# Kernel tuning notes

Hardware: AMD Instinct MI355X
Metric: run time of the kernel (lower is better)

## Reference

```python
import jax, jax.numpy as jnp
import numpy as np

N_HEAD = 8
D_HEAD = 64
D_MODEL = 512
CTX = 64
B = 2
Q_LEN = 2048
T = Q_LEN + CTX - 1


def setup_inputs() -> dict:
    key = jax.random.key(0)
    ks = jax.random.split(key, 7)
    HD = N_HEAD * D_HEAD
    return {
        "x": jax.random.normal(ks[0], (B, T, D_MODEL), jnp.float32),
        "r": jax.random.normal(ks[1], (CTX, D_MODEL), jnp.float32),
        "Wkv": jax.random.normal(ks[2], (D_MODEL, 2 * HD), jnp.float32) * 0.02,
        "Wq": jax.random.normal(ks[3], (D_MODEL, HD), jnp.float32) * 0.02,
        "bq": jax.random.normal(ks[4], (HD,), jnp.float32) * 0.02,
        "Wr": jax.random.normal(ks[5], (D_MODEL, HD), jnp.float32) * 0.02,
        "Wo": jax.random.normal(ks[6], (HD, D_MODEL), jnp.float32) * 0.02,
    }


def reference(x, r, Wkv, Wq, bq, Wr, Wo):
    Bb, Tt, _ = x.shape
    C = r.shape[0]
    H, Dh = N_HEAD, D_HEAD
    q_len = Tt - C + 1
    scale = Dh ** -0.5

    kv = x @ Wkv                                  # [B, T, 2*H*Dh]
    k_all = kv[..., : H * Dh].reshape(Bb, Tt, H, Dh)
    v_all = kv[..., H * Dh:].reshape(Bb, Tt, H, Dh)

    # sliding windows (torch unfold(1, ctx, 1) equivalent)
    idx = jnp.arange(q_len)[:, None] + jnp.arange(C)[None, :]   # [q, C]
    k_win = k_all[:, idx]                         # [B, q, C, H, Dh]
    v_win = v_all[:, idx]                         # [B, q, C, H, Dh]

    hq = (x[:, C - 1:] @ Wq + bq).reshape(Bb, q_len, H, Dh)     # [B, q, H, Dh]
    hr = (r @ Wr).reshape(C, H, Dh)                              # [C, H, Dh]

    # q . (k + r): split into content term + relative-position bias term
    scores = (jnp.einsum('bqhd,bqchd->bhqc', hq, k_win)
              + jnp.einsum('bqhd,chd->bhqc', hq, hr)) * scale    # [B, H, q, C]

    # padding mask: positions in first ctx-1 steps that are all-zero
    pad_mask = jnp.all(x[:, : C - 1] == 0, axis=-1)              # [B, C-1]
    full_mask = jnp.concatenate(
        [pad_mask, jnp.zeros((Bb, q_len), dtype=bool)], axis=1)  # [B, T]
    mask_win = full_mask[:, idx]                                 # [B, q, C]
    scores = jnp.where(mask_win[:, None], -jnp.inf, scores)

    w = jax.nn.softmax(scores, axis=-1)                          # [B, H, q, C]
    out = jnp.einsum('bhqc,bqchd->bqhd', w, v_win).reshape(Bb, q_len, H * Dh)
    return out @ Wo                                              # [B, q, d_model]
```

## Files before the change

### kernel.cpp

```cpp
#include <hip/hip_runtime.h>
#include <cstdint>
#include <cstddef>

#define NH 8
#define DH 64
#define DM 512
#define CTX 64
#define BB 2
#define QL 2048
#define TT (QL + CTX - 1)
#define HDIM 512
#define KVN 1024
#define KD 512

typedef unsigned short u16;
typedef __attribute__((ext_vector_type(8))) short bf16x8;
typedef __attribute__((ext_vector_type(4))) float f32x4;

__device__ __forceinline__ u16 f2bf(float f) {
    uint32_t u = __float_as_uint(f);
    u += 0x7FFF + ((u >> 16) & 1);
    return (u16)(u >> 16);
}
__device__ __forceinline__ uint32_t packbf(float lo, float hi) {
    return (uint32_t)f2bf(lo) | ((uint32_t)f2bf(hi) << 16);
}

#define GLLDS(g, l) __builtin_amdgcn_global_load_lds( \
    (const __attribute__((address_space(1))) void*)(g), \
    (__attribute__((address_space(3))) void*)(l), 16, 0, 0)

__global__ __launch_bounds__(256) void prep_kernel(
    const float* __restrict__ Wkv, const float* __restrict__ Wq,
    const float* __restrict__ Wr, const float* __restrict__ Wo,
    u16* __restrict__ WkvqT, u16* __restrict__ WrT, u16* __restrict__ WoT)
{
    __shared__ float tile[64][65];
    const int bid = blockIdx.x;
    const int tid = threadIdx.x;

    const float* W; u16* WT; int N; int tidx;
    if (bid < 128)      { W = Wkv; WT = WkvqT;                    N = 1024; tidx = bid; }
    else if (bid < 192) { W = Wq;  WT = WkvqT + (size_t)1024*512; N = 512;  tidx = bid - 128; }
    else if (bid < 256) { W = Wr;  WT = WrT;                      N = 512;  tidx = bid - 192; }
    else                { W = Wo;  WT = WoT;                      N = 512;  tidx = bid - 256; }
    const int tpr = N / 64;
    const int kb = (tidx / tpr) * 64, nb = (tidx % tpr) * 64;
    const int c4 = (tid & 15) * 4;
    for (int kk = tid >> 4; kk < 64; kk += 16) {
        float4 v = *(const float4*)&W[(size_t)(kb + kk) * N + nb + c4];
        tile[kk][c4 + 0] = v.x; tile[kk][c4 + 1] = v.y;
        tile[kk][c4 + 2] = v.z; tile[kk][c4 + 3] = v.w;
    }
    __syncthreads();
    for (int nn = tid >> 4; nn < 64; nn += 16) {
        ushort4 o;
        o.x = f2bf(tile[c4 + 0][nn]); o.y = f2bf(tile[c4 + 1][nn]);
        o.z = f2bf(tile[c4 + 2][nn]); o.w = f2bf(tile[c4 + 3][nn]);
        *(ushort4*)&WT[(size_t)(nb + nn) * KD + kb + c4] = o;
    }
}

__global__ __launch_bounds__(256) void gemm_fused(
    const float* __restrict__ x, const u16* __restrict__ WkvqT,
    u16* __restrict__ kvb, u16* __restrict__ hqb, const float* __restrict__ bq,
    const float* __restrict__ r, const u16* __restrict__ WrT,
    u16* __restrict__ hrb, float* __restrict__ maskv)
{
    const int bid = blockIdx.x;
    const int tid = threadIdx.x;

    if (bid >= 800) {
        __shared__ int anyflag;
        int idx = bid - 800;
        int t = idx >> 1, b = idx & 1;
        const float* row = x + (size_t)(b * TT + t) * DM;
        bool nz = (row[tid] != 0.f) || (row[tid + 256] != 0.f);
        if (tid == 0) anyflag = 0;
        __syncthreads();
        unsigned long long bal = __ballot(nz);
        if ((tid & 63) == 0 && bal) atomicOr(&anyflag, 1);
        __syncthreads();
        if (tid == 0) maskv[b * 64 + t] = anyflag ? 0.f : -1e30f;
        return;
    }

    __shared__ __align__(16) u16 As[2][128 * 32];
    __shared__ __align__(16) u16 Bs[2][64 * 32];

    const int lane = tid & 63;
    const int w    = tid >> 6;
    const int wm   = w * 32;

    const bool g3 = (bid >= 792);
    const float* A; const u16* BT; int m0, n0, mrows;
    if (g3) { A = r; BT = WrT;   m0 = 0;                n0 = (bid - 792) * 64; mrows = CTX; }
    else    { A = x; BT = WkvqT; m0 = (bid / 24) * 128; n0 = (bid % 24) * 64;  mrows = BB * TT; }

    const int arow = tid >> 1;
    const int akh  = (tid & 1) * 16;
    int grow = m0 + arow; if (grow >= mrows) grow = 0;
    const float* gA = A + (size_t)grow * KD + akh;

    const int bn0 = tid >> 2;
    const int bk0 = (tid & 3) * 8;
    const u16* gb0 = BT + (size_t)(n0 + bn0) * KD + bk0;

    float4 f0, f1, f2, f3;
#define ALOAD1(kt) do { \
    f0 = *(const float4*)(gA + (kt));      f1 = *(const float4*)(gA + (kt) + 4); \
    f2 = *(const float4*)(gA + (kt) + 8);  f3 = *(const float4*)(gA + (kt) + 12); \
} while (0)
#define AWRITE1(buf) do { \
    uint4 p0, p1; \
    p0.x = packbf(f0.x, f0.y); p0.y = packbf(f0.z, f0.w); \
    p0.z = packbf(f1.x, f1.y); p0.w = packbf(f1.z, f1.w); \
    p1.x = packbf(f2.x, f2.y); p1.y = packbf(f2.z, f2.w); \
    p1.z = packbf(f3.x, f3.y); p1.w = packbf(f3.z, f3.w); \
    *(uint4*)&As[buf][arow * 32 + akh]     = p0; \
    *(uint4*)&As[buf][arow * 32 + akh + 8] = p1; \
} while (0)
#define BSTAGE1(buf, kt) GLLDS(gb0 + (kt), &Bs[buf][(size_t)w * 512])

    f32x4 acc[2][4];
#pragma unroll
    for (int i = 0; i < 2; i++)
#pragma unroll
        for (int j = 0; j < 4; j++)
            acc[i][j] = (f32x4){0.f, 0.f, 0.f, 0.f};

    ALOAD1(0);
    AWRITE1(0);
    BSTAGE1(0, 0);
    __syncthreads();

    int cur = 0;
    const int fm = lane & 15;
    const int fk = (lane >> 4) * 8;
    for (int kt = 0; kt < KD; kt += 32) {
        const bool more = (kt + 32 < KD);
        if (more) { ALOAD1(kt + 32); BSTAGE1(cur ^ 1, kt + 32); }

        bf16x8 af[2], bfr[4];
#pragma unroll
        for (int i = 0; i < 2; i++)
            af[i] = *(const bf16x8*)&As[cur][(wm + i * 16 + fm) * 32 + fk];
#pragma unroll
        for (int j = 0; j < 4; j++)
            bfr[j] = *(const bf16x8*)&Bs[cur][(j * 16 + fm) * 32 + fk];
#pragma unroll
        for (int i = 0; i < 2; i++)
#pragma unroll
            for (int j = 0; j < 4; j++)
                acc[i][j] = __builtin_amdgcn_mfma_f32_16x16x32_bf16(af[i], bfr[j], acc[i][j], 0, 0, 0);

        if (more) AWRITE1(cur ^ 1);
        __syncthreads();
        cur ^= 1;
    }
#undef ALOAD1
#undef AWRITE1
#undef BSTAGE1

    const int fc = lane & 15;
    const int fr = (lane >> 4) * 4;
    if (!g3) {
        const bool iskv = (n0 < 1024);
#pragma unroll
        for (int i = 0; i < 2; i++)
#pragma unroll
            for (int rr = 0; rr < 4; rr++) {
                int row = m0 + wm + i * 16 + fr + rr;
                if (row < BB * TT) {
                    if (iskv) {
#pragma unroll
                        for (int j = 0; j < 4; j++) {
                            int col = n0 + j * 16 + fc;
                            kvb[(size_t)row * KVN + col] = f2bf(acc[i][j][rr]);
                        }
                    } else {
                        int bb = row / TT;
                        int t  = row - bb * TT;
                        if (t >= CTX - 1) {
                            size_t orow = (size_t)(bb * QL + t - (CTX - 1));
#pragma unroll
                            for (int j = 0; j < 4; j++) {
                                int col = n0 + j * 16 + fc - 1024;
                                hqb[orow * HDIM + col] = f2bf(acc[i][j][rr] + bq[col]);
                            }
                        }
                    }
                }
            }
    } else {
#pragma unroll
        for (int i = 0; i < 2; i++)
#pragma unroll
            for (int rr = 0; rr < 4; rr++) {
                int row = m0 + wm + i * 16 + fr + rr;
                if (row < CTX) {
#pragma unroll
                    for (int j = 0; j < 4; j++) {
                        int col = n0 + j * 16 + fc;
                        hrb[(size_t)row * HDIM + col] = f2bf(acc[i][j][rr]);
                    }
                }
            }
    }
}

__global__ __launch_bounds__(256, 4) void attn_mfma(
    const u16* __restrict__ kvb, const u16* __restrict__ hqb,
    const u16* __restrict__ hrb, const float* __restrict__ maskv,
    u16* __restrict__ attnb)
{
    __shared__ __align__(16) char lds[37888];
    float* sprime = (float*)lds;
    u16*   vTs    = (u16*)lds;
    u16*   wband  = (u16*)(lds + 20480);

    const int q0 = blockIdx.x * 64;
    const int h  = blockIdx.y;
    const int b  = blockIdx.z;
    const int tid  = threadIdx.x;
    const int lane = tid & 63;
    const int w    = tid >> 6;
    const int qb   = q0 + w * 16;

    const int vr0 = tid >> 4;
    const int vc4 = (tid & 15) * 4;
    ushort4 vreg[8];
#pragma unroll
    for (int i = 0; i < 8; i++) {
        int rr = vr0 + i * 16;
        if (rr < 127)
            vreg[i] = *(const ushort4*)&kvb[(size_t)(b * TT + q0 + rr) * KVN + HDIM + h * DH + vc4];
        else
            vreg[i] = (ushort4){0, 0, 0, 0};
    }

    {
        uint32_t* wz = (uint32_t*)wband;
#pragma unroll
        for (int i = 0; i < 17; i++) wz[tid + i * 256] = 0;
    }
    asm volatile("s_waitcnt lgkmcnt(0)" ::: "memory");
    __builtin_amdgcn_s_barrier();

    const int fm = lane & 15;
    const int fk = (lane >> 4) * 8;

    const u16* hqrow = hqb + (size_t)(b * QL + qb + fm) * HDIM + h * DH + fk;
// ... 64 lines not shown
    __syncthreads();

#pragma unroll
    for (int i = 0; i < 8; i++) {
        int rr = vr0 + i * 16;
        vTs[(vc4 + 0) * 136 + rr] = vreg[i].x;
        vTs[(vc4 + 1) * 136 + rr] = vreg[i].y;
        vTs[(vc4 + 2) * 136 + rr] = vreg[i].z;
        vTs[(vc4 + 3) * 136 + rr] = vreg[i].w;
    }
    __syncthreads();

    f32x4 oacc[4];
#pragma unroll
    for (int j = 0; j < 4; j++) oacc[j] = (f32x4){0.f, 0.f, 0.f, 0.f};
#pragma unroll
    for (int ks = 0; ks < 4; ks++) {
        bf16x8 wa = *(const bf16x8*)&wband[(w * 16 + fm) * 136 + ks * 32 + fk];
#pragma unroll
        for (int j = 0; j < 4; j++) {
            bf16x8 vb = *(const bf16x8*)&vTs[(j * 16 + fm) * 136 + ks * 32 + fk];
            oacc[j] = __builtin_amdgcn_mfma_f32_16x16x32_bf16(wa, vb, oacc[j], 0, 0, 0);
        }
    }
    {
        const int row = (lane >> 4) * 4;
#pragma unroll
        for (int j = 0; j < 4; j++)
#pragma unroll
            for (int r2 = 0; r2 < 4; r2++)
                attnb[(size_t)(b * QL + qb + row + r2) * HDIM + h * DH + j * 16 + fm] =
                    f2bf(oacc[j][r2]);
    }
}

__global__ __launch_bounds__(256) void gemm_n64(
    const u16* __restrict__ A, const u16* __restrict__ BT,
    float* __restrict__ C)
{
    __shared__ u16 As[2][64 * 32];
    __shared__ u16 Bs[2][64 * 32];

    const int tid  = threadIdx.x;
    const int lane = tid & 63;
    const int w    = tid >> 6;
    const int wm   = (w >> 1) * 32;
    const int wn   = (w & 1) * 32;
    const int m0   = (blockIdx.x >> 3) * 64;
    const int n0   = (blockIdx.x & 7) * 64;

    const int am0 = tid >> 2;
    const int ak0 = (tid & 3) * 8;
    const u16* ga0 = A  + (size_t)(m0 + am0) * KD + ak0;
    const u16* gb0 = BT + (size_t)(n0 + am0) * KD + ak0;

    f32x4 acc[2][2];
#pragma unroll
    for (int i = 0; i < 2; i++)
#pragma unroll
        for (int j = 0; j < 2; j++)
            acc[i][j] = (f32x4){0.f, 0.f, 0.f, 0.f};

    GLLDS(ga0, &As[0][(size_t)w * 512]);
    GLLDS(gb0, &Bs[0][(size_t)w * 512]);
    __syncthreads();

    int cur = 0;
    const int fm = lane & 15;
    const int fk = (lane >> 4) * 8;
    for (int kt = 0; kt < KD; kt += 32) {
        if (kt + 32 < KD) {
            GLLDS(ga0 + kt + 32, &As[cur ^ 1][(size_t)w * 512]);
            GLLDS(gb0 + kt + 32, &Bs[cur ^ 1][(size_t)w * 512]);
        }
        bf16x8 af[2], bfr[2];
#pragma unroll
        for (int i = 0; i < 2; i++)
            af[i] = *(const bf16x8*)&As[cur][(wm + i * 16 + fm) * 32 + fk];
#pragma unroll
        for (int j = 0; j < 2; j++)
            bfr[j] = *(const bf16x8*)&Bs[cur][(wn + j * 16 + fm) * 32 + fk];
#pragma unroll
        for (int i = 0; i < 2; i++)
#pragma unroll
            for (int j = 0; j < 2; j++)
                acc[i][j] = __builtin_amdgcn_mfma_f32_16x16x32_bf16(af[i], bfr[j], acc[i][j], 0, 0, 0);
        __syncthreads();
        cur ^= 1;
    }

    const int fc = lane & 15;
    const int fr = (lane >> 4) * 4;
#pragma unroll
    for (int i = 0; i < 2; i++)
#pragma unroll
        for (int rr = 0; rr < 4; rr++) {
            int row = m0 + wm + i * 16 + fr + rr;
#pragma unroll
            for (int j = 0; j < 2; j++) {
                int col = n0 + wn + j * 16 + fc;
                C[(size_t)row * HDIM + col] = acc[i][j][rr];
            }
        }
}

extern "C" void kernel_launch(void* const* d_in, const int* in_sizes, int n_in,
                              void* d_out, int out_size, void* d_ws, size_t ws_size,
                              hipStream_t stream)
{
    const float* x   = (const float*)d_in[0];
    const float* r   = (const float*)d_in[1];
    const float* Wkv = (const float*)d_in[2];
    const float* Wq  = (const float*)d_in[3];
    const float* bq  = (const float*)d_in[4];
    const float* Wr  = (const float*)d_in[5];
    const float* Wo  = (const float*)d_in[6];
    float* out = (float*)d_out;

    char* p = (char*)d_ws;
    u16* WkvqT  = (u16*)p;  p += (size_t)1536 * 512 * 2;
    u16* WrT    = (u16*)p;  p += (size_t)512 * 512 * 2;
    u16* WoT    = (u16*)p;  p += (size_t)512 * 512 * 2;
    u16* kvb    = (u16*)p;  p += (size_t)4224 * 1024 * 2;
    u16* hqb    = (u16*)p;  p += (size_t)4096 * 512 * 2;
    u16* hrb    = (u16*)p;  p += (size_t)64 * 512 * 2;
    u16* attnb  = (u16*)p;  p += (size_t)4096 * 512 * 2;
    float* maskv = (float*)p;

    hipLaunchKernelGGL(prep_kernel, dim3(320), dim3(256), 0, stream,
                       Wkv, Wq, Wr, Wo, WkvqT, WrT, WoT);
    hipLaunchKernelGGL(gemm_fused, dim3(928), dim3(256), 0, stream,
                       x, WkvqT, kvb, hqb, bq, r, WrT, hrb, maskv);
    hipLaunchKernelGGL(attn_mfma, dim3(QL / 64, NH, BB), dim3(256), 0, stream,
                       kvb, hqb, hrb, maskv, attnb);
    hipLaunchKernelGGL(gemm_n64, dim3(512), dim3(256), 0, stream,
                       attnb, WoT, out);
}
```

Before: 125.4 us.

## Drop weight prep kernel and fuse output projection into attention via counters

Removes the weight transpose/convert prep kernel; the projection GEMM now reads fp32 weights directly and converts them to bf16 while staging into padded LDS. The separate Wo GEMM kernel is removed: each attention block bumps a per-(batch, q-block) atomic counter, and the last of the 8 head blocks computes the 64x512 output projection for that row tile from attnb and fp32 Wo. This cuts two launches and an intermediate pass, at the cost of the output GEMM running on only 64 blocks with serialized tails, redundant fp32 weight conversion in every block, and the launch_bounds occupancy hint being dropped from the attention kernel.

```diff
diff --git a/kernel.cpp b/kernel.cpp
--- a/kernel.cpp
+++ b/kernel.cpp
@@ -30,42 +30,12 @@
     (const __attribute__((address_space(1))) void*)(g), \
     (__attribute__((address_space(3))) void*)(l), 16, 0, 0)
 
-__global__ __launch_bounds__(256) void prep_kernel(
-    const float* __restrict__ Wkv, const float* __restrict__ Wq,
-    const float* __restrict__ Wr, const float* __restrict__ Wo,
-    u16* __restrict__ WkvqT, u16* __restrict__ WrT, u16* __restrict__ WoT)
-{
-    __shared__ float tile[64][65];
-    const int bid = blockIdx.x;
-    const int tid = threadIdx.x;
-
-    const float* W; u16* WT; int N; int tidx;
-    if (bid < 128)      { W = Wkv; WT = WkvqT;                    N = 1024; tidx = bid; }
-    else if (bid < 192) { W = Wq;  WT = WkvqT + (size_t)1024*512; N = 512;  tidx = bid - 128; }
-    else if (bid < 256) { W = Wr;  WT = WrT;                      N = 512;  tidx = bid - 192; }
-    else                { W = Wo;  WT = WoT;                      N = 512;  tidx = bid - 256; }
-    const int tpr = N / 64;
-    const int kb = (tidx / tpr) * 64, nb = (tidx % tpr) * 64;
-    const int c4 = (tid & 15) * 4;
-    for (int kk = tid >> 4; kk < 64; kk += 16) {
-        float4 v = *(const float4*)&W[(size_t)(kb + kk) * N + nb + c4];
-        tile[kk][c4 + 0] = v.x; tile[kk][c4 + 1] = v.y;
-        tile[kk][c4 + 2] = v.z; tile[kk][c4 + 3] = v.w;
-    }
-    __syncthreads();
-    for (int nn = tid >> 4; nn < 64; nn += 16) {
-        ushort4 o;
-        o.x = f2bf(tile[c4 + 0][nn]); o.y = f2bf(tile[c4 + 1][nn]);
-        o.z = f2bf(tile[c4 + 2][nn]); o.w = f2bf(tile[c4 + 3][nn]);
-        *(ushort4*)&WT[(size_t)(nb + nn) * KD + kb + c4] = o;
-    }
-}
-
 __global__ __launch_bounds__(256) void gemm_fused(
-    const float* __restrict__ x, const u16* __restrict__ WkvqT,
-    u16* __restrict__ kvb, u16* __restrict__ hqb, const float* __restrict__ bq,
-    const float* __restrict__ r, const u16* __restrict__ WrT,
-    u16* __restrict__ hrb, float* __restrict__ maskv)
+    const float* __restrict__ x, const float* __restrict__ Wkv,
+    const float* __restrict__ Wq, const float* __restrict__ bq,
+    const float* __restrict__ r, const float* __restrict__ Wr,
+    u16* __restrict__ kvb, u16* __restrict__ hqb, u16* __restrict__ hrb,
+    float* __restrict__ maskv, int* __restrict__ ctrs)
 {
     const int bid = blockIdx.x;
     const int tid = threadIdx.x;
@@ -73,6 +43,7 @@
     if (bid >= 800) {
         __shared__ int anyflag;
         int idx = bid - 800;
+        if (idx == 0 && tid < 64) ctrs[tid] = 0;
         int t = idx >> 1, b = idx & 1;
         const float* row = x + (size_t)(b * TT + t) * DM;
         bool nz = (row[tid] != 0.f) || (row[tid + 256] != 0.f);
@@ -86,27 +57,34 @@
     }
 
     __shared__ __align__(16) u16 As[2][128 * 32];
-    __shared__ __align__(16) u16 Bs[2][64 * 32];
+    __shared__ __align__(16) u16 Bs[2][64 * 40];
 
     const int lane = tid & 63;
     const int w    = tid >> 6;
     const int wm   = w * 32;
 
     const bool g3 = (bid >= 792);
-    const float* A; const u16* BT; int m0, n0, mrows;
-    if (g3) { A = r; BT = WrT;   m0 = 0;                n0 = (bid - 792) * 64; mrows = CTX; }
-    else    { A = x; BT = WkvqT; m0 = (bid / 24) * 128; n0 = (bid % 24) * 64;  mrows = BB * TT; }
+    const float* A; const float* Bw; int ldb, coln, m0, n0, mrows;
+    if (g3) {
+        A = r; m0 = 0; n0 = (bid - 792) * 64; mrows = CTX;
+        Bw = Wr; ldb = 512; coln = n0;
+    } else {
+        A = x; m0 = (bid / 24) * 128; n0 = (bid % 24) * 64; mrows = BB * TT;
+        if (n0 < 1024) { Bw = Wkv; ldb = 1024; coln = n0; }
+        else           { Bw = Wq;  ldb = 512;  coln = n0 - 1024; }
+    }
 
     const int arow = tid >> 1;
     const int akh  = (tid & 1) * 16;
     int grow = m0 + arow; if (grow >= mrows) grow = 0;
     const float* gA = A + (size_t)grow * KD + akh;
 
-    const int bn0 = tid >> 2;
-    const int bk0 = (tid & 3) * 8;
-    const u16* gb0 = BT + (size_t)(n0 + bn0) * KD + bk0;
-
-    float4 f0, f1, f2, f3;
+    const int kkp = tid & 15;
+    const int c4n = (tid >> 4) * 4;
+    const float* gB0 = Bw + (size_t)(2 * kkp) * ldb + coln + c4n;
+    const float* gB1 = gB0 + ldb;
+
+    float4 f0, f1, f2, f3, ba, bb;
 #define ALOAD1(kt) do { \
     f0 = *(const float4*)(gA + (kt));      f1 = *(const float4*)(gA + (kt) + 4); \
     f2 = *(const float4*)(gA + (kt) + 8);  f3 = *(const float4*)(gA + (kt) + 12); \
@@ -120,7 +98,17 @@
     *(uint4*)&As[buf][arow * 32 + akh]     = p0; \
     *(uint4*)&As[buf][arow * 32 + akh + 8] = p1; \
 } while (0)
-#define BSTAGE1(buf, kt) GLLDS(gb0 + (kt), &Bs[buf][(size_t)w * 512])
+#define BLOAD1(kt) do { \
+    ba = *(const float4*)(gB0 + (size_t)(kt) * ldb); \
+    bb = *(const float4*)(gB1 + (size_t)(kt) * ldb); \
+} while (0)
+#define BWRITE1(buf) do { \
+    uint32_t* d = (uint32_t*)&Bs[buf][0]; \
+    d[(c4n + 0) * 20 + kkp] = packbf(ba.x, bb.x); \
+    d[(c4n + 1) * 20 + kkp] = packbf(ba.y, bb.y); \
+    d[(c4n + 2) * 20 + kkp] = packbf(ba.z, bb.z); \
+    d[(c4n + 3) * 20 + kkp] = packbf(ba.w, bb.w); \
+} while (0)
 
     f32x4 acc[2][4];
 #pragma unroll
@@ -129,9 +117,8 @@
         for (int j = 0; j < 4; j++)
             acc[i][j] = (f32x4){0.f, 0.f, 0.f, 0.f};
 
-    ALOAD1(0);
-    AWRITE1(0);
-    BSTAGE1(0, 0);
+    ALOAD1(0); BLOAD1(0);
+    AWRITE1(0); BWRITE1(0);
     __syncthreads();
 
     int cur = 0;
@@ -139,7 +126,7 @@
     const int fk = (lane >> 4) * 8;
     for (int kt = 0; kt < KD; kt += 32) {
         const bool more = (kt + 32 < KD);
-        if (more) { ALOAD1(kt + 32); BSTAGE1(cur ^ 1, kt + 32); }
+        if (more) { ALOAD1(kt + 32); BLOAD1(kt + 32); }
 
         bf16x8 af[2], bfr[4];
 #pragma unroll
@@ -147,20 +134,21 @@
             af[i] = *(const bf16x8*)&As[cur][(wm + i * 16 + fm) * 32 + fk];
 #pragma unroll
         for (int j = 0; j < 4; j++)
-            bfr[j] = *(const bf16x8*)&Bs[cur][(j * 16 + fm) * 32 + fk];
+            bfr[j] = *(const bf16x8*)&Bs[cur][(j * 16 + fm) * 40 + fk];
 #pragma unroll
         for (int i = 0; i < 2; i++)
 #pragma unroll
             for (int j = 0; j < 4; j++)
                 acc[i][j] = __builtin_amdgcn_mfma_f32_16x16x32_bf16(af[i], bfr[j], acc[i][j], 0, 0, 0);
 
-        if (more) AWRITE1(cur ^ 1);
+        if (more) { AWRITE1(cur ^ 1); BWRITE1(cur ^ 1); }
         __syncthreads();
         cur ^= 1;
     }
 #undef ALOAD1
 #undef AWRITE1
-#undef BSTAGE1
+#undef BLOAD1
+#undef BWRITE1
 
     const int fc = lane & 15;
     const int fr = (lane >> 4) * 4;
@@ -179,10 +167,10 @@
                             kvb[(size_t)row * KVN + col] = f2bf(acc[i][j][rr]);
                         }
                     } else {
-                        int bb = row / TT;
-                        int t  = row - bb * TT;
+                        int bb2 = row / TT;
+                        int t   = row - bb2 * TT;
                         if (t >= CTX - 1) {
-                            size_t orow = (size_t)(bb * QL + t - (CTX - 1));
+                            size_t orow = (size_t)(bb2 * QL + t - (CTX - 1));
 #pragma unroll
                             for (int j = 0; j < 4; j++) {
                                 int col = n0 + j * 16 + fc - 1024;
@@ -209,12 +197,14 @@
     }
 }
 
-__global__ __launch_bounds__(256, 4) void attn_mfma(
+__global__ __launch_bounds__(256) void attn_mfma(
     const u16* __restrict__ kvb, const u16* __restrict__ hqb,
     const u16* __restrict__ hrb, const float* __restrict__ maskv,
-    u16* __restrict__ attnb)
+    u16* __restrict__ attnb, const float* __restrict__ Wo,
+    float* __restrict__ out, int* __restrict__ ctrs)
 {
     __shared__ __align__(16) char lds[37888];
+    __shared__ int lastflag;
     float* sprime = (float*)lds;
     u16*   vTs    = (u16*)lds;
     u16*   wband  = (u16*)(lds + 20480);
@@ -348,76 +338,114 @@
                 attnb[(size_t)(b * QL + qb + row + r2) * HDIM + h * DH + j * 16 + fm] =
                     f2bf(oacc[j][r2]);
     }
-}
-
-__global__ __launch_bounds__(256) void gemm_n64(
-    const u16* __restrict__ A, const u16* __restrict__ BT,
-    float* __restrict__ C)
-{
-    __shared__ u16 As[2][64 * 32];
-    __shared__ u16 Bs[2][64 * 32];
-
-    const int tid  = threadIdx.x;
-    const int lane = tid & 63;
-    const int w    = tid >> 6;
-    const int wm   = (w >> 1) * 32;
-    const int wn   = (w & 1) * 32;
-    const int m0   = (blockIdx.x >> 3) * 64;
-    const int n0   = (blockIdx.x & 7) * 64;
-
-    const int am0 = tid >> 2;
-    const int ak0 = (tid & 3) * 8;
-    const u16* ga0 = A  + (size_t)(m0 + am0) * KD + ak0;
-    const u16* gb0 = BT + (size_t)(n0 + am0) * KD + ak0;
-
-    f32x4 acc[2][2];
-#pragma unroll
-    for (int i = 0; i < 2; i++)
-#pragma unroll
-        for (int j = 0; j < 2; j++)
-            acc[i][j] = (f32x4){0.f, 0.f, 0.f, 0.f};
-
-    GLLDS(ga0, &As[0][(size_t)w * 512]);
-    GLLDS(gb0, &Bs[0][(size_t)w * 512]);
+
+    __threadfence();
     __syncthreads();
-
-    int cur = 0;
-    const int fm = lane & 15;
-    const int fk = (lane >> 4) * 8;
-    for (int kt = 0; kt < KD; kt += 32) {
-        if (kt + 32 < KD) {
-            GLLDS(ga0 + kt + 32, &As[cur ^ 1][(size_t)w * 512]);
-            GLLDS(gb0 + kt + 32, &Bs[cur ^ 1][(size_t)w * 512]);
+    if (tid == 0) {
+        int old = atomicAdd(&ctrs[b * 32 + blockIdx.x], 1);
+        lastflag = (old == 7);
+    }
+    __syncthreads();
+    if (!lastflag) return;
+    __threadfence();
+
+    {
+        u16 (*As2)[64 * 32] = (u16 (*)[64 * 32])lds;
+        uint32_t* Bs2U = (uint32_t*)(lds + 8192);
+        u16* Bs2 = (u16*)Bs2U;
+
+        const int rb0 = b * QL + q0;
+        const int am0 = tid >> 2;
+        const int ak0 = (tid & 3) * 8;
+        const u16* gA2 = attnb + (size_t)(rb0 + am0) * HDIM + ak0;
+        const int kkp = tid & 15;
+        const int c4n = (tid >> 4) * 4;
+
+        const int wm2 = (w & 1) * 32;
+        const int wn2 = (w >> 1) * 128;
+        const int fc = lane & 15;
+        const int fr = (lane >> 4) * 4;
+
+        for (int nh = 0; nh < 2; nh++) {
+            const float* wb = Wo + (size_t)(2 * kkp) * DM + nh * 256 + c4n;
+            float4 a0, b0, a1, b1, a2, b2, a3, b3;
+#define B2LOAD(kt) do { \
+    a0 = *(const float4*)(wb + (size_t)(kt) * DM);        b0 = *(const float4*)(wb + (size_t)(kt) * DM + DM); \
+    a1 = *(const float4*)(wb + (size_t)(kt) * DM + 64);   b1 = *(const float4*)(wb + (size_t)(kt) * DM + DM + 64); \
+    a2 = *(const float4*)(wb + (size_t)(kt) * DM + 128);  b2 = *(const float4*)(wb + (size_t)(kt) * DM + DM + 128); \
+    a3 = *(const float4*)(wb + (size_t)(kt) * DM + 192);  b3 = *(const float4*)(wb + (size_t)(kt) * DM + DM + 192); \
+} while (0)
+#define B2WRITE() do { \
+    Bs2U[(c4n + 0) * 20 + kkp]         = packbf(a0.x, b0.x); \
+    Bs2U[(c4n + 1) * 20 + kkp]         = packbf(a0.y, b0.y); \
+    Bs2U[(c4n + 2) * 20 + kkp]         = packbf(a0.z, b0.z); \
+    Bs2U[(c4n + 3) * 20 + kkp]         = packbf(a0.w, b0.w); \
+    Bs2U[(64 + c4n + 0) * 20 + kkp]    = packbf(a1.x, b1.x); \
+    Bs2U[(64 + c4n + 1) * 20 + kkp]    = packbf(a1.y, b1.y); \
+    Bs2U[(64 + c4n + 2) * 20 + kkp]    = packbf(a1.z, b1.z); \
+    Bs2U[(64 + c4n + 3) * 20 + kkp]    = packbf(a1.w, b1.w); \
+    Bs2U[(128 + c4n + 0) * 20 + kkp]   = packbf(a2.x, b2.x); \
+    Bs2U[(128 + c4n + 1) * 20 + kkp]   = packbf(a2.y, b2.y); \
+    Bs2U[(128 + c4n + 2) * 20 + kkp]   = packbf(a2.z, b2.z); \
+    Bs2U[(128 + c4n + 3) * 20 + kkp]   = packbf(a2.w, b2.w); \
+    Bs2U[(192 + c4n + 0) * 20 + kkp]   = packbf(a3.x, b3.x); \
+    Bs2U[(192 + c4n + 1) * 20 + kkp]   = packbf(a3.y, b3.y); \
+    Bs2U[(192 + c4n + 2) * 20 + kkp]   = packbf(a3.z, b3.z); \
+    Bs2U[(192 + c4n + 3) * 20 + kkp]   = packbf(a3.w, b3.w); \
+} while (0)
+
+            f32x4 acc2[2][8];
+#pragma unroll
+            for (int i = 0; i < 2; i++)
+#pragma unroll
+                for (int j = 0; j < 8; j++)
+                    acc2[i][j] = (f32x4){0.f, 0.f, 0.f, 0.f};
+
+            B2LOAD(0);
+            GLLDS(gA2, &As2[0][(size_t)w * 512]);
+            B2WRITE();
+            __syncthreads();
+
+            int cur2 = 0;
+            for (int kt = 0; kt < KD; kt += 32) {
+                const bool more = (kt + 32 < KD);
+                if (more) {
+                    GLLDS(gA2 + kt + 32, &As2[cur2 ^ 1][(size_t)w * 512]);
+                    B2LOAD(kt + 32);
+                }
+                bf16x8 af2[2];
+#pragma unroll
+                for (int i = 0; i < 2; i++)
+                    af2[i] = *(const bf16x8*)&As2[cur2][(wm2 + i * 16 + fm) * 32 + fk];
+#pragma unroll
+                for (int j = 0; j < 8; j++) {
+                    bf16x8 bf2 = *(const bf16x8*)&Bs2[(wn2 + j * 16 + fm) * 40 + fk];
+#pragma unroll
+                    for (int i = 0; i < 2; i++)
+                        acc2[i][j] = __builtin_amdgcn_mfma_f32_16x16x32_bf16(af2[i], bf2, acc2[i][j], 0, 0, 0);
+                }
+                __syncthreads();
+                if (more) B2WRITE();
+                __syncthreads();
+                cur2 ^= 1;
+            }
+#undef B2LOAD
+#undef B2WRITE
+
+#pragma unroll
+            for (int i = 0; i < 2; i++)
+#pragma unroll
+                for (int rr = 0; rr < 4; rr++) {
+                    int row = rb0 + wm2 + i * 16 + fr + rr;
+#pragma unroll
+                    for (int j = 0; j < 8; j++) {
+                        int col = nh * 256 + wn2 + j * 16 + fc;
+                        out[(size_t)row * DM + col] = acc2[i][j][rr];
+                    }
+                }
+            __syncthreads();
         }
-        bf16x8 af[2], bfr[2];
-#pragma unroll
-        for (int i = 0; i < 2; i++)
-            af[i] = *(const bf16x8*)&As[cur][(wm + i * 16 + fm) * 32 + fk];
-#pragma unroll
-        for (int j = 0; j < 2; j++)
-            bfr[j] = *(const bf16x8*)&Bs[cur][(wn + j * 16 + fm) * 32 + fk];
-#pragma unroll
-        for (int i = 0; i < 2; i++)
-#pragma unroll
-            for (int j = 0; j < 2; j++)
-                acc[i][j] = __builtin_amdgcn_mfma_f32_16x16x32_bf16(af[i], bfr[j], acc[i][j], 0, 0, 0);
-        __syncthreads();
-        cur ^= 1;
-    }
-
-    const int fc = lane & 15;
-    const int fr = (lane >> 4) * 4;
-#pragma unroll
-    for (int i = 0; i < 2; i++)
-#pragma unroll
-        for (int rr = 0; rr < 4; rr++) {
-            int row = m0 + wm + i * 16 + fr + rr;
-#pragma unroll
-            for (int j = 0; j < 2; j++) {
-                int col = n0 + wn + j * 16 + fc;
-                C[(size_t)row * HDIM + col] = acc[i][j][rr];
-            }
-        }
+    }
 }
 
 extern "C" void kernel_launch(void* const* d_in, const int* in_sizes, int n_in,
@@ -434,21 +462,15 @@
     float* out = (float*)d_out;
 
     char* p = (char*)d_ws;
-    u16* WkvqT  = (u16*)p;  p += (size_t)1536 * 512 * 2;
-    u16* WrT    = (u16*)p;  p += (size_t)512 * 512 * 2;
-    u16* WoT    = (u16*)p;  p += (size_t)512 * 512 * 2;
     u16* kvb    = (u16*)p;  p += (size_t)4224 * 1024 * 2;
     u16* hqb    = (u16*)p;  p += (size_t)4096 * 512 * 2;
     u16* hrb    = (u16*)p;  p += (size_t)64 * 512 * 2;
     u16* attnb  = (u16*)p;  p += (size_t)4096 * 512 * 2;
-    float* maskv = (float*)p;
-
-    hipLaunchKernelGGL(prep_kernel, dim3(320), dim3(256), 0, stream,
-                       Wkv, Wq, Wr, Wo, WkvqT, WrT, WoT);
+    float* maskv = (float*)p; p += 128 * sizeof(float);
+    int* ctrs   = (int*)p;
+
     hipLaunchKernelGGL(gemm_fused, dim3(928), dim3(256), 0, stream,
-                       x, WkvqT, kvb, hqb, bq, r, WrT, hrb, maskv);
+                       x, Wkv, Wq, bq, r, Wr, kvb, hqb, hrb, maskv, ctrs);
     hipLaunchKernelGGL(attn_mfma, dim3(QL / 64, NH, BB), dim3(256), 0, stream,
-                       kvb, hqb, hrb, maskv, attnb);
-    hipLaunchKernelGGL(gemm_n64, dim3(512), dim3(256), 0, stream,
-                       attnb, WoT, out);
+                       kvb, hqb, hrb, maskv, attnb, Wo, out, ctrs);
 }
```

Measured after the change: 241.8 us. 92.7% more time.

## Fuse weight prep into projection GEMM and Wo GEMM into attention via counters

Applied to the files above, without the earlier changes.

Merges the weight transpose/convert kernel into the projection GEMM kernel. GEMM blocks spin on per-slice atomic counters until their weight slices are ready. The output projection is folded into the attention kernel: the 8 head blocks for a query tile meet at an atomic counter, then each computes one 64-column slice of the Wo product. This cuts four launches to two plus a memset and lets the stages overlap. The cost is spin-waiting that relies on producer blocks being scheduled ahead of their consumers. The waits are capped by iteration limits, so correctness depends on dispatch order. Attention also loses its occupancy hint of 4.

```diff
diff --git a/kernel.cpp b/kernel.cpp
--- a/kernel.cpp
+++ b/kernel.cpp
@@ -30,49 +30,51 @@
     (const __attribute__((address_space(1))) void*)(g), \
     (__attribute__((address_space(3))) void*)(l), 16, 0, 0)
 
-__global__ __launch_bounds__(256) void prep_kernel(
+__global__ __launch_bounds__(256) void front_kernel(
+    const float* __restrict__ x, const float* __restrict__ r,
     const float* __restrict__ Wkv, const float* __restrict__ Wq,
-    const float* __restrict__ Wr, const float* __restrict__ Wo,
-    u16* __restrict__ WkvqT, u16* __restrict__ WrT, u16* __restrict__ WoT)
-{
-    __shared__ float tile[64][65];
-    const int bid = blockIdx.x;
-    const int tid = threadIdx.x;
-
-    const float* W; u16* WT; int N; int tidx;
-    if (bid < 128)      { W = Wkv; WT = WkvqT;                    N = 1024; tidx = bid; }
-    else if (bid < 192) { W = Wq;  WT = WkvqT + (size_t)1024*512; N = 512;  tidx = bid - 128; }
-    else if (bid < 256) { W = Wr;  WT = WrT;                      N = 512;  tidx = bid - 192; }
-    else                { W = Wo;  WT = WoT;                      N = 512;  tidx = bid - 256; }
-    const int tpr = N / 64;
-    const int kb = (tidx / tpr) * 64, nb = (tidx % tpr) * 64;
-    const int c4 = (tid & 15) * 4;
-    for (int kk = tid >> 4; kk < 64; kk += 16) {
-        float4 v = *(const float4*)&W[(size_t)(kb + kk) * N + nb + c4];
-        tile[kk][c4 + 0] = v.x; tile[kk][c4 + 1] = v.y;
-        tile[kk][c4 + 2] = v.z; tile[kk][c4 + 3] = v.w;
-    }
-    __syncthreads();
-    for (int nn = tid >> 4; nn < 64; nn += 16) {
-        ushort4 o;
-        o.x = f2bf(tile[c4 + 0][nn]); o.y = f2bf(tile[c4 + 1][nn]);
-        o.z = f2bf(tile[c4 + 2][nn]); o.w = f2bf(tile[c4 + 3][nn]);
-        *(ushort4*)&WT[(size_t)(nb + nn) * KD + kb + c4] = o;
-    }
-}
-
-__global__ __launch_bounds__(256) void gemm_fused(
-    const float* __restrict__ x, const u16* __restrict__ WkvqT,
-    u16* __restrict__ kvb, u16* __restrict__ hqb, const float* __restrict__ bq,
-    const float* __restrict__ r, const u16* __restrict__ WrT,
-    u16* __restrict__ hrb, float* __restrict__ maskv)
+    const float* __restrict__ bq, const float* __restrict__ Wr,
+    const float* __restrict__ Wo,
+    u16* __restrict__ WkvqT, u16* __restrict__ WrT, u16* __restrict__ WoT,
+    u16* __restrict__ kvb, u16* __restrict__ hqb, u16* __restrict__ hrb,
+    float* __restrict__ maskv, int* __restrict__ ctrs)
 {
     const int bid = blockIdx.x;
     const int tid = threadIdx.x;
-
-    if (bid >= 800) {
+    int* wctr = ctrs;
+
+    if (bid < 320) {
+        __shared__ float tile[64][65];
+        const float* W; u16* WT; int N; int tidx; int slice;
+        if (bid < 128)      { W = Wkv; WT = WkvqT;                    N = 1024; tidx = bid;       slice = tidx % 16; }
+        else if (bid < 192) { W = Wq;  WT = WkvqT + (size_t)1024*512; N = 512;  tidx = bid - 128; slice = 16 + tidx % 8; }
+        else if (bid < 256) { W = Wr;  WT = WrT;                      N = 512;  tidx = bid - 192; slice = 24 + tidx % 8; }
+        else                { W = Wo;  WT = WoT;                      N = 512;  tidx = bid - 256; slice = -1; }
+        const int tpr = N / 64;
+        const int kb = (tidx / tpr) * 64, nb = (tidx % tpr) * 64;
+        const int c4 = (tid & 15) * 4;
+        for (int kk = tid >> 4; kk < 64; kk += 16) {
+            float4 v = *(const float4*)&W[(size_t)(kb + kk) * N + nb + c4];
+            tile[kk][c4 + 0] = v.x; tile[kk][c4 + 1] = v.y;
+            tile[kk][c4 + 2] = v.z; tile[kk][c4 + 3] = v.w;
+        }
+        __syncthreads();
+        for (int nn = tid >> 4; nn < 64; nn += 16) {
+            ushort4 o;
+            o.x = f2bf(tile[c4 + 0][nn]); o.y = f2bf(tile[c4 + 1][nn]);
+            o.z = f2bf(tile[c4 + 2][nn]); o.w = f2bf(tile[c4 + 3][nn]);
+            *(ushort4*)&WT[(size_t)(nb + nn) * KD + kb + c4] = o;
+        }
+        if (slice >= 0) {
+            __threadfence();
+            __syncthreads();
+            if (tid == 0) atomicAdd(&wctr[slice], 1);
+        }
+        return;
+    }
+    if (bid < 448) {
         __shared__ int anyflag;
-        int idx = bid - 800;
+        int idx = bid - 320;
         int t = idx >> 1, b = idx & 1;
         const float* row = x + (size_t)(b * TT + t) * DM;
         bool nz = (row[tid] != 0.f) || (row[tid + 256] != 0.f);
@@ -88,14 +90,15 @@
     __shared__ __align__(16) u16 As[2][128 * 32];
     __shared__ __align__(16) u16 Bs[2][64 * 32];
 
+    const int gbid = bid - 448;
     const int lane = tid & 63;
     const int w    = tid >> 6;
     const int wm   = w * 32;
 
-    const bool g3 = (bid >= 792);
-    const float* A; const u16* BT; int m0, n0, mrows;
-    if (g3) { A = r; BT = WrT;   m0 = 0;                n0 = (bid - 792) * 64; mrows = CTX; }
-    else    { A = x; BT = WkvqT; m0 = (bid / 24) * 128; n0 = (bid % 24) * 64;  mrows = BB * TT; }
+    const bool g3 = (gbid >= 792);
+    const float* A; const u16* BT; int m0, n0, mrows, slice;
+    if (g3) { A = r; BT = WrT;   m0 = 0;                  n0 = (gbid - 792) * 64; mrows = CTX;     slice = 24 + (n0 >> 6); }
+    else    { A = x; BT = WkvqT; m0 = (gbid / 24) * 128;  n0 = (gbid % 24) * 64;  mrows = BB * TT; slice = gbid % 24; }
 
     const int arow = tid >> 1;
     const int akh  = (tid & 1) * 16;
@@ -122,6 +125,17 @@
 } while (0)
 #define BSTAGE1(buf, kt) GLLDS(gb0 + (kt), &Bs[buf][(size_t)w * 512])
 
+    ALOAD1(0);
+    if (tid == 0) {
+        int it = 0;
+        while (__hip_atomic_load(&wctr[slice], __ATOMIC_ACQUIRE,
+                                 __HIP_MEMORY_SCOPE_AGENT) < 8 && it < 200000) {
+            __builtin_amdgcn_s_sleep(16); ++it;
+        }
+    }
+    __syncthreads();
+    __threadfence();
+
     f32x4 acc[2][4];
 #pragma unroll
     for (int i = 0; i < 2; i++)
@@ -129,7 +143,6 @@
         for (int j = 0; j < 4; j++)
             acc[i][j] = (f32x4){0.f, 0.f, 0.f, 0.f};
 
-    ALOAD1(0);
     AWRITE1(0);
     BSTAGE1(0, 0);
     __syncthreads();
@@ -179,10 +192,10 @@
                             kvb[(size_t)row * KVN + col] = f2bf(acc[i][j][rr]);
                         }
                     } else {
-                        int bb = row / TT;
-                        int t  = row - bb * TT;
+                        int bb2 = row / TT;
+                        int t   = row - bb2 * TT;
                         if (t >= CTX - 1) {
-                            size_t orow = (size_t)(bb * QL + t - (CTX - 1));
+                            size_t orow = (size_t)(bb2 * QL + t - (CTX - 1));
 #pragma unroll
                             for (int j = 0; j < 4; j++) {
                                 int col = n0 + j * 16 + fc - 1024;
@@ -209,15 +222,17 @@
     }
 }
 
-__global__ __launch_bounds__(256, 4) void attn_mfma(
+__global__ __launch_bounds__(256) void attn_g2(
     const u16* __restrict__ kvb, const u16* __restrict__ hqb,
     const u16* __restrict__ hrb, const float* __restrict__ maskv,
-    u16* __restrict__ attnb)
+    u16* __restrict__ attnb, const u16* __restrict__ WoT,
+    float* __restrict__ out, int* __restrict__ ctrs)
 {
     __shared__ __align__(16) char lds[37888];
     float* sprime = (float*)lds;
     u16*   vTs    = (u16*)lds;
     u16*   wband  = (u16*)(lds + 20480);
+    int* actr = ctrs + 32;
 
     const int q0 = blockIdx.x * 64;
     const int h  = blockIdx.y;
@@ -348,76 +363,81 @@
                 attnb[(size_t)(b * QL + qb + row + r2) * HDIM + h * DH + j * 16 + fm] =
                     f2bf(oacc[j][r2]);
     }
-}
-
-__global__ __launch_bounds__(256) void gemm_n64(
-    const u16* __restrict__ A, const u16* __restrict__ BT,
-    float* __restrict__ C)
-{
-    __shared__ u16 As[2][64 * 32];
-    __shared__ u16 Bs[2][64 * 32];
-
-    const int tid  = threadIdx.x;
-    const int lane = tid & 63;
-    const int w    = tid >> 6;
-    const int wm   = (w >> 1) * 32;
-    const int wn   = (w & 1) * 32;
-    const int m0   = (blockIdx.x >> 3) * 64;
-    const int n0   = (blockIdx.x & 7) * 64;
-
-    const int am0 = tid >> 2;
-    const int ak0 = (tid & 3) * 8;
-    const u16* ga0 = A  + (size_t)(m0 + am0) * KD + ak0;
-    const u16* gb0 = BT + (size_t)(n0 + am0) * KD + ak0;
-
-    f32x4 acc[2][2];
-#pragma unroll
-    for (int i = 0; i < 2; i++)
-#pragma unroll
-        for (int j = 0; j < 2; j++)
-            acc[i][j] = (f32x4){0.f, 0.f, 0.f, 0.f};
-
-    GLLDS(ga0, &As[0][(size_t)w * 512]);
-    GLLDS(gb0, &Bs[0][(size_t)w * 512]);
-    __syncthreads();
-
-    int cur = 0;
-    const int fm = lane & 15;
-    const int fk = (lane >> 4) * 8;
-    for (int kt = 0; kt < KD; kt += 32) {
-        if (kt + 32 < KD) {
-            GLLDS(ga0 + kt + 32, &As[cur ^ 1][(size_t)w * 512]);
-            GLLDS(gb0 + kt + 32, &Bs[cur ^ 1][(size_t)w * 512]);
-        }
-        bf16x8 af[2], bfr[2];
-#pragma unroll
-        for (int i = 0; i < 2; i++)
-            af[i] = *(const bf16x8*)&As[cur][(wm + i * 16 + fm) * 32 + fk];
-#pragma unroll
-        for (int j = 0; j < 2; j++)
-            bfr[j] = *(const bf16x8*)&Bs[cur][(wn + j * 16 + fm) * 32 + fk];
+
+    __threadfence();
+    __syncthreads();
+    if (tid == 0) {
+        atomicAdd(&actr[b * 32 + blockIdx.x], 1);
+        int it = 0;
+        while (__hip_atomic_load(&actr[b * 32 + blockIdx.x], __ATOMIC_ACQUIRE,
+                                 __HIP_MEMORY_SCOPE_AGENT) < 8 && it < 200000) {
+            __builtin_amdgcn_s_sleep(16); ++it;
+        }
+    }
+    __syncthreads();
+    __threadfence();
+
+    {
+        u16 (*As2)[64 * 32] = (u16 (*)[64 * 32])lds;
+        u16 (*Bs2)[64 * 32] = (u16 (*)[64 * 32])(lds + 8192);
+
+        const int m0 = b * QL + q0;
+        const int n0 = h * 64;
+        const int wm2 = (w >> 1) * 32;
+        const int wn2 = (w & 1) * 32;
+
+        const int am0 = tid >> 2;
+        const int ak0 = (tid & 3) * 8;
+        const u16* ga0 = attnb + (size_t)(m0 + am0) * HDIM + ak0;
+        const u16* gb0 = WoT   + (size_t)(n0 + am0) * KD + ak0;
+
+        f32x4 acc2[2][2];
 #pragma unroll
         for (int i = 0; i < 2; i++)
 #pragma unroll
             for (int j = 0; j < 2; j++)
-                acc[i][j] = __builtin_amdgcn_mfma_f32_16x16x32_bf16(af[i], bfr[j], acc[i][j], 0, 0, 0);
+                acc2[i][j] = (f32x4){0.f, 0.f, 0.f, 0.f};
+
+        GLLDS(ga0, &As2[0][(size_t)w * 512]);
+        GLLDS(gb0, &Bs2[0][(size_t)w * 512]);
         __syncthreads();
-        cur ^= 1;
-    }
-
-    const int fc = lane & 15;
-    const int fr = (lane >> 4) * 4;
-#pragma unroll
-    for (int i = 0; i < 2; i++)
-#pragma unroll
-        for (int rr = 0; rr < 4; rr++) {
-            int row = m0 + wm + i * 16 + fr + rr;
-#pragma unroll
-            for (int j = 0; j < 2; j++) {
-                int col = n0 + wn + j * 16 + fc;
-                C[(size_t)row * HDIM + col] = acc[i][j][rr];
+
+        int cur2 = 0;
+        for (int kt = 0; kt < KD; kt += 32) {
+            if (kt + 32 < KD) {
+                GLLDS(ga0 + kt + 32, &As2[cur2 ^ 1][(size_t)w * 512]);
+                GLLDS(gb0 + kt + 32, &Bs2[cur2 ^ 1][(size_t)w * 512]);
             }
-        }
+            bf16x8 af2[2], bf2[2];
+#pragma unroll
+            for (int i = 0; i < 2; i++)
+                af2[i] = *(const bf16x8*)&As2[cur2][(wm2 + i * 16 + fm) * 32 + fk];
+#pragma unroll
+            for (int j = 0; j < 2; j++)
+                bf2[j] = *(const bf16x8*)&Bs2[cur2][(wn2 + j * 16 + fm) * 32 + fk];
+#pragma unroll
+            for (int i = 0; i < 2; i++)
+#pragma unroll
+                for (int j = 0; j < 2; j++)
+                    acc2[i][j] = __builtin_amdgcn_mfma_f32_16x16x32_bf16(af2[i], bf2[j], acc2[i][j], 0, 0, 0);
+            __syncthreads();
+            cur2 ^= 1;
+        }
+
+        const int fc = lane & 15;
+        const int fr = (lane >> 4) * 4;
+#pragma unroll
+        for (int i = 0; i < 2; i++)
+#pragma unroll
+            for (int rr = 0; rr < 4; rr++) {
+                int row = m0 + wm2 + i * 16 + fr + rr;
+#pragma unroll
+                for (int j = 0; j < 2; j++) {
+                    int col = n0 + wn2 + j * 16 + fc;
+                    out[(size_t)row * DM + col] = acc2[i][j][rr];
+                }
+            }
+    }
 }
 
 extern "C" void kernel_launch(void* const* d_in, const int* in_sizes, int n_in,
@@ -441,14 +461,13 @@
     u16* hqb    = (u16*)p;  p += (size_t)4096 * 512 * 2;
     u16* hrb    = (u16*)p;  p += (size_t)64 * 512 * 2;
     u16* attnb  = (u16*)p;  p += (size_t)4096 * 512 * 2;
-    float* maskv = (float*)p;
-
-    hipLaunchKernelGGL(prep_kernel, dim3(320), dim3(256), 0, stream,
-                       Wkv, Wq, Wr, Wo, WkvqT, WrT, WoT);
-    hipLaunchKernelGGL(gemm_fused, dim3(928), dim3(256), 0, stream,
-                       x, WkvqT, kvb, hqb, bq, r, WrT, hrb, maskv);
-    hipLaunchKernelGGL(attn_mfma, dim3(QL / 64, NH, BB), dim3(256), 0, stream,
-                       kvb, hqb, hrb, maskv, attnb);
-    hipLaunchKernelGGL(gemm_n64, dim3(512), dim3(256), 0, stream,
-                       attnb, WoT, out);
+    float* maskv = (float*)p; p += 128 * sizeof(float);
+    int* ctrs   = (int*)p;
+
+    hipMemsetAsync(ctrs, 0, 96 * sizeof(int), stream);
+    hipLaunchKernelGGL(front_kernel, dim3(1248), dim3(256), 0, stream,
+                       x, r, Wkv, Wq, bq, Wr, Wo,
+                       WkvqT, WrT, WoT, kvb, hqb, hrb, maskv, ctrs);
+    hipLaunchKernelGGL(attn_g2, dim3(QL / 64, NH, BB), dim3(256), 0, stream,
+                       kvb, hqb, hrb, maskv, attnb, WoT, out, ctrs);
 }
```

Result: slower. 344.1 us (+174.3%).

## Fold weight transpose and bf16 conversion into GEMM B-tile loading

Applied to the files above, without the earlier changes.

Drops the separate prep kernel that transposed and converted all weight matrices to bf16. The GEMM kernels now read fp32 weights directly, pack pairs of k rows into bf16 and write them transposed into a padded LDS tile (stride 20 words). This removes one launch and a full pass over the weights, but it replaces async global-to-LDS loads for B with register loads plus scattered LDS stores. Every GEMM block now repeats the weight conversion.

```diff
diff --git a/kernel.cpp b/kernel.cpp
--- a/kernel.cpp
+++ b/kernel.cpp
@@ -30,42 +30,12 @@
     (const __attribute__((address_space(1))) void*)(g), \
     (__attribute__((address_space(3))) void*)(l), 16, 0, 0)
 
-__global__ __launch_bounds__(256) void prep_kernel(
-    const float* __restrict__ Wkv, const float* __restrict__ Wq,
-    const float* __restrict__ Wr, const float* __restrict__ Wo,
-    u16* __restrict__ WkvqT, u16* __restrict__ WrT, u16* __restrict__ WoT)
-{
-    __shared__ float tile[64][65];
-    const int bid = blockIdx.x;
-    const int tid = threadIdx.x;
-
-    const float* W; u16* WT; int N; int tidx;
-    if (bid < 128)      { W = Wkv; WT = WkvqT;                    N = 1024; tidx = bid; }
-    else if (bid < 192) { W = Wq;  WT = WkvqT + (size_t)1024*512; N = 512;  tidx = bid - 128; }
-    else if (bid < 256) { W = Wr;  WT = WrT;                      N = 512;  tidx = bid - 192; }
-    else                { W = Wo;  WT = WoT;                      N = 512;  tidx = bid - 256; }
-    const int tpr = N / 64;
-    const int kb = (tidx / tpr) * 64, nb = (tidx % tpr) * 64;
-    const int c4 = (tid & 15) * 4;
-    for (int kk = tid >> 4; kk < 64; kk += 16) {
-        float4 v = *(const float4*)&W[(size_t)(kb + kk) * N + nb + c4];
-        tile[kk][c4 + 0] = v.x; tile[kk][c4 + 1] = v.y;
-        tile[kk][c4 + 2] = v.z; tile[kk][c4 + 3] = v.w;
-    }
-    __syncthreads();
-    for (int nn = tid >> 4; nn < 64; nn += 16) {
-        ushort4 o;
-        o.x = f2bf(tile[c4 + 0][nn]); o.y = f2bf(tile[c4 + 1][nn]);
-        o.z = f2bf(tile[c4 + 2][nn]); o.w = f2bf(tile[c4 + 3][nn]);
-        *(ushort4*)&WT[(size_t)(nb + nn) * KD + kb + c4] = o;
-    }
-}
-
 __global__ __launch_bounds__(256) void gemm_fused(
-    const float* __restrict__ x, const u16* __restrict__ WkvqT,
-    u16* __restrict__ kvb, u16* __restrict__ hqb, const float* __restrict__ bq,
-    const float* __restrict__ r, const u16* __restrict__ WrT,
-    u16* __restrict__ hrb, float* __restrict__ maskv)
+    const float* __restrict__ x, const float* __restrict__ Wkv,
+    const float* __restrict__ Wq, const float* __restrict__ bq,
+    const float* __restrict__ r, const float* __restrict__ Wr,
+    u16* __restrict__ kvb, u16* __restrict__ hqb, u16* __restrict__ hrb,
+    float* __restrict__ maskv)
 {
     const int bid = blockIdx.x;
     const int tid = threadIdx.x;
@@ -86,27 +56,34 @@
     }
 
     __shared__ __align__(16) u16 As[2][128 * 32];
-    __shared__ __align__(16) u16 Bs[2][64 * 32];
+    __shared__ __align__(16) uint32_t BsU[2][64 * 20];
 
     const int lane = tid & 63;
     const int w    = tid >> 6;
     const int wm   = w * 32;
 
     const bool g3 = (bid >= 792);
-    const float* A; const u16* BT; int m0, n0, mrows;
-    if (g3) { A = r; BT = WrT;   m0 = 0;                n0 = (bid - 792) * 64; mrows = CTX; }
-    else    { A = x; BT = WkvqT; m0 = (bid / 24) * 128; n0 = (bid % 24) * 64;  mrows = BB * TT; }
+    const float* A; const float* Bw; int ldb, coln, m0, n0, mrows;
+    if (g3) {
+        A = r; m0 = 0; n0 = (bid - 792) * 64; mrows = CTX;
+        Bw = Wr; ldb = 512; coln = n0;
+    } else {
+        A = x; m0 = (bid / 24) * 128; n0 = (bid % 24) * 64; mrows = BB * TT;
+        if (n0 < 1024) { Bw = Wkv; ldb = 1024; coln = n0; }
+        else           { Bw = Wq;  ldb = 512;  coln = n0 - 1024; }
+    }
 
     const int arow = tid >> 1;
     const int akh  = (tid & 1) * 16;
     int grow = m0 + arow; if (grow >= mrows) grow = 0;
     const float* gA = A + (size_t)grow * KD + akh;
 
-    const int bn0 = tid >> 2;
-    const int bk0 = (tid & 3) * 8;
-    const u16* gb0 = BT + (size_t)(n0 + bn0) * KD + bk0;
-
-    float4 f0, f1, f2, f3;
+    const int kkp = tid >> 4;
+    const int nj  = (tid & 15) * 4;
+    const float* gB0 = Bw + (size_t)(2 * kkp) * ldb + coln + nj;
+    const float* gB1 = gB0 + ldb;
+
+    float4 f0, f1, f2, f3, ba, bb;
 #define ALOAD1(kt) do { \
     f0 = *(const float4*)(gA + (kt));      f1 = *(const float4*)(gA + (kt) + 4); \
     f2 = *(const float4*)(gA + (kt) + 8);  f3 = *(const float4*)(gA + (kt) + 12); \
@@ -120,7 +97,16 @@
     *(uint4*)&As[buf][arow * 32 + akh]     = p0; \
     *(uint4*)&As[buf][arow * 32 + akh + 8] = p1; \
 } while (0)
-#define BSTAGE1(buf, kt) GLLDS(gb0 + (kt), &Bs[buf][(size_t)w * 512])
+#define BLOAD1(kt) do { \
+    ba = *(const float4*)(gB0 + (size_t)(kt) * ldb); \
+    bb = *(const float4*)(gB1 + (size_t)(kt) * ldb); \
+} while (0)
+#define BWRITE1(buf) do { \
+    BsU[buf][(nj + 0) * 20 + kkp] = packbf(ba.x, bb.x); \
+    BsU[buf][(nj + 1) * 20 + kkp] = packbf(ba.y, bb.y); \
+    BsU[buf][(nj + 2) * 20 + kkp] = packbf(ba.z, bb.z); \
+    BsU[buf][(nj + 3) * 20 + kkp] = packbf(ba.w, bb.w); \
+} while (0)
 
     f32x4 acc[2][4];
 #pragma unroll
@@ -129,9 +115,8 @@
         for (int j = 0; j < 4; j++)
             acc[i][j] = (f32x4){0.f, 0.f, 0.f, 0.f};
 
-    ALOAD1(0);
-    AWRITE1(0);
-    BSTAGE1(0, 0);
+    ALOAD1(0); BLOAD1(0);
+    AWRITE1(0); BWRITE1(0);
     __syncthreads();
 
     int cur = 0;
@@ -139,28 +124,30 @@
     const int fk = (lane >> 4) * 8;
     for (int kt = 0; kt < KD; kt += 32) {
         const bool more = (kt + 32 < KD);
-        if (more) { ALOAD1(kt + 32); BSTAGE1(cur ^ 1, kt + 32); }
-
+        if (more) { ALOAD1(kt + 32); BLOAD1(kt + 32); }
+
+        const u16* Bs16 = (const u16*)&BsU[cur][0];
         bf16x8 af[2], bfr[4];
 #pragma unroll
         for (int i = 0; i < 2; i++)
             af[i] = *(const bf16x8*)&As[cur][(wm + i * 16 + fm) * 32 + fk];
 #pragma unroll
         for (int j = 0; j < 4; j++)
-            bfr[j] = *(const bf16x8*)&Bs[cur][(j * 16 + fm) * 32 + fk];
+            bfr[j] = *(const bf16x8*)&Bs16[(j * 16 + fm) * 40 + fk];
 #pragma unroll
         for (int i = 0; i < 2; i++)
 #pragma unroll
             for (int j = 0; j < 4; j++)
                 acc[i][j] = __builtin_amdgcn_mfma_f32_16x16x32_bf16(af[i], bfr[j], acc[i][j], 0, 0, 0);
 
-        if (more) AWRITE1(cur ^ 1);
+        if (more) { AWRITE1(cur ^ 1); BWRITE1(cur ^ 1); }
         __syncthreads();
         cur ^= 1;
     }
 #undef ALOAD1
 #undef AWRITE1
-#undef BSTAGE1
+#undef BLOAD1
+#undef BWRITE1
 
     const int fc = lane & 15;
     const int fr = (lane >> 4) * 4;
@@ -179,10 +166,10 @@
                             kvb[(size_t)row * KVN + col] = f2bf(acc[i][j][rr]);
                         }
                     } else {
-                        int bb = row / TT;
-                        int t  = row - bb * TT;
+                        int bb2 = row / TT;
+                        int t   = row - bb2 * TT;
                         if (t >= CTX - 1) {
-                            size_t orow = (size_t)(bb * QL + t - (CTX - 1));
+                            size_t orow = (size_t)(bb2 * QL + t - (CTX - 1));
 #pragma unroll
                             for (int j = 0; j < 4; j++) {
                                 int col = n0 + j * 16 + fc - 1024;
@@ -351,11 +338,11 @@
 }
 
 __global__ __launch_bounds__(256) void gemm_n64(
-    const u16* __restrict__ A, const u16* __restrict__ BT,
+    const u16* __restrict__ A, const float* __restrict__ Wo,
     float* __restrict__ C)
 {
-    __shared__ u16 As[2][64 * 32];
-    __shared__ u16 Bs[2][64 * 32];
+    __shared__ __align__(16) u16 As[2][64 * 32];
+    __shared__ __align__(16) uint32_t BsU[2][64 * 20];
 
     const int tid  = threadIdx.x;
     const int lane = tid & 63;
@@ -367,8 +354,24 @@
 
     const int am0 = tid >> 2;
     const int ak0 = (tid & 3) * 8;
-    const u16* ga0 = A  + (size_t)(m0 + am0) * KD + ak0;
-    const u16* gb0 = BT + (size_t)(n0 + am0) * KD + ak0;
+    const u16* ga0 = A + (size_t)(m0 + am0) * KD + ak0;
+
+    const int kkp = tid >> 4;
+    const int nj  = (tid & 15) * 4;
+    const float* gB0 = Wo + (size_t)(2 * kkp) * DM + n0 + nj;
+    const float* gB1 = gB0 + DM;
+
+    float4 ba, bb;
+#define BLOAD2(kt) do { \
+    ba = *(const float4*)(gB0 + (size_t)(kt) * DM); \
+    bb = *(const float4*)(gB1 + (size_t)(kt) * DM); \
+} while (0)
+#define BWRITE2(buf) do { \
+    BsU[buf][(nj + 0) * 20 + kkp] = packbf(ba.x, bb.x); \
+    BsU[buf][(nj + 1) * 20 + kkp] = packbf(ba.y, bb.y); \
+    BsU[buf][(nj + 2) * 20 + kkp] = packbf(ba.z, bb.z); \
+    BsU[buf][(nj + 3) * 20 + kkp] = packbf(ba.w, bb.w); \
+} while (0)
 
     f32x4 acc[2][2];
 #pragma unroll
@@ -377,33 +380,40 @@
         for (int j = 0; j < 2; j++)
             acc[i][j] = (f32x4){0.f, 0.f, 0.f, 0.f};
 
+    BLOAD2(0);
     GLLDS(ga0, &As[0][(size_t)w * 512]);
-    GLLDS(gb0, &Bs[0][(size_t)w * 512]);
+    BWRITE2(0);
     __syncthreads();
 
     int cur = 0;
     const int fm = lane & 15;
     const int fk = (lane >> 4) * 8;
     for (int kt = 0; kt < KD; kt += 32) {
-        if (kt + 32 < KD) {
+        const bool more = (kt + 32 < KD);
+        if (more) {
             GLLDS(ga0 + kt + 32, &As[cur ^ 1][(size_t)w * 512]);
-            GLLDS(gb0 + kt + 32, &Bs[cur ^ 1][(size_t)w * 512]);
-        }
-        bf16x8 af[2], bfr[2];
-#pragma unroll
-        for (int i = 0; i < 2; i++)
-            af[i] = *(const bf16x8*)&As[cur][(wm + i * 16 + fm) * 32 + fk];
+            BLOAD2(kt + 32);
+        }
+        const u16* Bs16 = (const u16*)&BsU[cur][0];
+        bf16x8 af2[2], bf2[2];
+#pragma unroll
+        for (int i = 0; i < 2; i++)
+            af2[i] = *(const bf16x8*)&As[cur][(wm + i * 16 + fm) * 32 + fk];
 #pragma unroll
         for (int j = 0; j < 2; j++)
-            bfr[j] = *(const bf16x8*)&Bs[cur][(wn + j * 16 + fm) * 32 + fk];
+            bf2[j] = *(const bf16x8*)&Bs16[(wn + j * 16 + fm) * 40 + fk];
 #pragma unroll
         for (int i = 0; i < 2; i++)
 #pragma unroll
             for (int j = 0; j < 2; j++)
-                acc[i][j] = __builtin_amdgcn_mfma_f32_16x16x32_bf16(af[i], bfr[j], acc[i][j], 0, 0, 0);
+                acc[i][j] = __builtin_amdgcn_mfma_f32_16x16x32_bf16(af2[i], bf2[j], acc[i][j], 0, 0, 0);
+
+        if (more) BWRITE2(cur ^ 1);
         __syncthreads();
         cur ^= 1;
     }
+#undef BLOAD2
+#undef BWRITE2
 
     const int fc = lane & 15;
     const int fr = (lane >> 4) * 4;
@@ -415,7 +425,7 @@
 #pragma unroll
             for (int j = 0; j < 2; j++) {
                 int col = n0 + wn + j * 16 + fc;
-                C[(size_t)row * HDIM + col] = acc[i][j][rr];
+                C[(size_t)row * DM + col] = acc[i][j][rr];
             }
         }
 }
@@ -434,21 +444,16 @@
     float* out = (float*)d_out;
 
     char* p = (char*)d_ws;
-    u16* WkvqT  = (u16*)p;  p += (size_t)1536 * 512 * 2;
-    u16* WrT    = (u16*)p;  p += (size_t)512 * 512 * 2;
-    u16* WoT    = (u16*)p;  p += (size_t)512 * 512 * 2;
     u16* kvb    = (u16*)p;  p += (size_t)4224 * 1024 * 2;
     u16* hqb    = (u16*)p;  p += (size_t)4096 * 512 * 2;
     u16* hrb    = (u16*)p;  p += (size_t)64 * 512 * 2;
     u16* attnb  = (u16*)p;  p += (size_t)4096 * 512 * 2;
     float* maskv = (float*)p;
 
-    hipLaunchKernelGGL(prep_kernel, dim3(320), dim3(256), 0, stream,
-                       Wkv, Wq, Wr, Wo, WkvqT, WrT, WoT);
     hipLaunchKernelGGL(gemm_fused, dim3(928), dim3(256), 0, stream,
-                       x, WkvqT, kvb, hqb, bq, r, WrT, hrb, maskv);
+                       x, Wkv, Wq, bq, r, Wr, kvb, hqb, hrb, maskv);
     hipLaunchKernelGGL(attn_mfma, dim3(QL / 64, NH, BB), dim3(256), 0, stream,
                        kvb, hqb, hrb, maskv, attnb);
     hipLaunchKernelGGL(gemm_n64, dim3(512), dim3(256), 0, stream,
-                       attnb, WoT, out);
-}
+                       attnb, Wo, out);
+}
```

Result: faster. 123.0 us (median of 2 runs) (-2.0%).
